# Performance work log

Measured on AMD Instinct MI355X. Metric: run time of the kernel, lower is better.

Reference implementation:

```python
import jax, jax.numpy as jnp
import numpy as np
from jax import lax

B, T = 16, 1000
IN_DIM = 257
CTX = 3            # left + 1 + right
FEAT = CTX * IN_DIM  # 771
H = 512
L = 2              # SRU layers
KN = 9             # conv kernels
KS = 6             # conv kernel size


def setup_inputs() -> dict:
    key = jax.random.key(0)
    ks = jax.random.split(key, 10)
    n = jax.random.normal
    return {
        "inputs": n(ks[0], (B, T, FEAT), jnp.float32),
        "W_in": n(ks[1], (FEAT, H), jnp.float32) / np.sqrt(FEAT),
        "b_in": jnp.zeros((H,), jnp.float32),
        "W_rnn": n(ks[2], (L, H, 3 * H), jnp.float32) / np.sqrt(H),
        "v_rnn": n(ks[3], (L, 2 * H), jnp.float32) * 0.1,
        "b_rnn": jnp.zeros((L, 2 * H), jnp.float32),
        "conv_k": n(ks[4], (KN, 1, KS, KS), jnp.float32) * 0.05,
        "conv_b": jnp.zeros((KN,), jnp.float32),
        "W_out": n(ks[5], (H * KN, FEAT), jnp.float32) / np.sqrt(H * KN),
        "b_out": jnp.zeros((FEAT,), jnp.float32),
    }


def _sru_layer(x, W, v, b):
    # x: (T, B, H) time-major; SRU: c_t = f_t*c_{t-1} + (1-f_t)*(W x_t),
    # highway h_t = r_t*c_t + (1-r_t)*x_t; gates peek at c_{t-1} via v.
    U = jnp.einsum("tbh,hk->tbk", x, W)          # (T, B, 3H)
    xt, fp, rp = jnp.split(U, 3, axis=-1)
    vf, vr = jnp.split(v, 2)
    bf, br = jnp.split(b, 2)

    def step(c, inp):
        xt_t, fp_t, rp_t, xin_t = inp
        f = jax.nn.sigmoid(fp_t + vf * c + bf)
        c_new = f * c + (1.0 - f) * xt_t
        r = jax.nn.sigmoid(rp_t + vr * c + br)
        h = r * c_new + (1.0 - r) * xin_t
        return c_new, h

    c0 = jnp.zeros(x.shape[1:], x.dtype)
    _, hs = lax.scan(step, c0, (xt, fp, rp, x))
    return hs


def reference(inputs, W_in, b_in, W_rnn, v_rnn, b_rnn, conv_k, conv_b, W_out, b_out):
    # input layer: Linear + Tanh
    h = jnp.tanh(jnp.einsum("btf,fh->bth", inputs, W_in) + b_in)  # (B,T,H)
    x = jnp.transpose(h, (1, 0, 2))                               # (T,B,H)
    for l in range(L):
        x = _sru_layer(x, W_rnn[l], v_rnn[l], b_rnn[l])
    h = jnp.transpose(x, (1, 0, 2))[:, None]                      # (B,1,T,H)

    # Conv2d with asymmetric pad (left/top 3, right/bottom 2), +bias, tanh
    y = lax.conv_general_dilated(
        h, conv_k, window_strides=(1, 1), padding=[(3, 2), (3, 2)],
        dimension_numbers=("NCHW", "OIHW", "NCHW"))
    y = jnp.tanh(y + conv_b[None, :, None, None])                 # (B,KN,T,H)
    # MaxPool2d(3, stride=1, padding=1)
    y = lax.reduce_window(y, -jnp.inf, lax.max, (1, 1, 3, 3), (1, 1, 1, 1),
                          [(0, 0), (0, 0), (1, 1), (1, 1)])

    # (B,KN,T,H) -> (B,T,H,KN) -> (B,T,H*KN)  (matches torch double transpose)
    y = jnp.transpose(y, (0, 2, 3, 1)).reshape(B, T, H * KN)
    mask = jax.nn.sigmoid(jnp.einsum("btf,fo->bto", y, W_out) + b_out)
    out = mask * inputs
    return out[:, :, IN_DIM:2 * IN_DIM]  # center frame (left_context slice)
```

## Files before the change

kernel.cpp:

```cpp
#include <hip/hip_runtime.h>
#include <hip/hip_bf16.h>

#define B_    16
#define T_    1000
#define FEAT  771
#define FEATP 800
#define H_    512
#define H3    1536
#define KN_   9
#define KHID  4608
#define M_    16000
#define NOUT  257
#define KSLICES 3

typedef _Float16 half8 __attribute__((ext_vector_type(8)));
typedef _Float16 half4 __attribute__((ext_vector_type(4)));
typedef _Float16 half2v __attribute__((ext_vector_type(2)));
typedef _Float16 h2 __attribute__((ext_vector_type(2)));
typedef float    floatx4 __attribute__((ext_vector_type(4)));

__device__ inline float tanh_fast(float z) {
    return 1.0f - 2.0f / (1.0f + __expf(2.0f * z));
}
__device__ inline float sigmoid_fast(float z) {
    return 1.0f / (1.0f + __expf(-z));
}

__device__ inline void gload16(const _Float16* g, _Float16* l) {
    __builtin_amdgcn_global_load_lds(
        (const __attribute__((address_space(1))) void*)g,
        (__attribute__((address_space(3))) void*)l, 16, 0, 0);
}

__device__ inline h2 pkfma(unsigned int w, unsigned int x, h2 c) {
    const h2 a = __builtin_bit_cast(h2, w);
    const h2 b = __builtin_bit_cast(h2, x);
#if __has_builtin(__builtin_elementwise_fma)
    return __builtin_elementwise_fma(a, b, c);
#else
    return a * b + c;
#endif
}

__global__ void convert_inputs(const float* __restrict__ in, _Float16* __restrict__ A1) {
    size_t i = (size_t)blockIdx.x * 256 + threadIdx.x;
    if (i >= (size_t)M_ * FEATP) return;
    size_t r = i / FEATP;
    int   cc = (int)(i % FEATP);
    A1[i] = (cc < FEAT) ? (_Float16)in[r * FEAT + cc] : (_Float16)0.f;
}

__global__ void pack_ck(const float* __restrict__ ck, unsigned int* __restrict__ ckp) {
    const int i = threadIdx.x;
    if (i < 9 * 36) {
        const _Float16 w = (_Float16)ck[i];
        const unsigned short u = __builtin_bit_cast(unsigned short, w);
        ckp[i] = ((unsigned int)u << 16) | u;
    }
}

__global__ __launch_bounds__(256) void transpose_w(
    const float* __restrict__ W, _Float16* __restrict__ Wt,
    int K, int N, int ldw, int coloff, int Kp, int perm9)
{
    __shared__ float tile[32][33];
    const int kb = blockIdx.x * 32;
    const int nb = blockIdx.y * 32;
    const int tx = threadIdx.x & 31;
    const int ty = threadIdx.x >> 5;
    #pragma unroll
    for (int r = ty; r < 32; r += 8) {
        const int k = kb + r, n = nb + tx;
        tile[r][tx] = (k < K && n < N) ? W[(size_t)k * ldw + coloff + n] : 0.f;
    }
    __syncthreads();
    #pragma unroll
    for (int r = ty; r < 32; r += 8) {
        const int n = nb + r, k = kb + tx;
        if (n < N && k < Kp) {
            size_t kidx = (size_t)k;
            if (perm9) kidx = (size_t)(k % 9) * 512 + (size_t)(k / 9);
            Wt[(size_t)n * Kp + kidx] = (_Float16)tile[tx][r];
        }
    }
}

template <int EPI>
__global__ __launch_bounds__(256) void gemm_kernel(
    const _Float16* __restrict__ A, const _Float16* __restrict__ Bt,
    int Kp, int nk, int Nb,
    _Float16* __restrict__ Ch, float* __restrict__ Cf, int ldc,
    const float* __restrict__ bias)
{
    __shared__ __align__(16) _Float16 As[128][32];
    __shared__ __align__(16) _Float16 Bs[128][32];

    const int tid  = threadIdx.x;
    const int m0   = blockIdx.x * 128;
    const int n0   = blockIdx.y * 128;
    const int koff = blockIdx.z * (nk << 5);
    const int wave = tid >> 6;
    const int lane = tid & 63;
    const int wr   = (wave >> 1) << 6;
    const int wc   = (wave & 1) << 6;
    const int lrow = lane & 15;
    const int lq   = lane >> 4;

    const int srow0  = wave * 32 + (lane >> 2);
    const int schunk = (lane & 3) * 8;
    const _Float16* aSrc = A  + (size_t)(m0 + srow0) * Kp + koff + schunk;
    const _Float16* bSrc = Bt + (size_t)(n0 + srow0) * Kp + koff + schunk;
    _Float16* aDst0 = &As[wave * 32][0];
    _Float16* aDst1 = &As[wave * 32 + 16][0];
    _Float16* bDst0 = &Bs[wave * 32][0];
    _Float16* bDst1 = &Bs[wave * 32 + 16][0];
    const size_t rstep = (size_t)16 * Kp;

    floatx4 acc[4][4];
    #pragma unroll
    for (int i = 0; i < 4; ++i)
        #pragma unroll
        for (int j = 0; j < 4; ++j)
            #pragma unroll
            for (int r = 0; r < 4; ++r) acc[i][j][r] = 0.f;

    for (int kc = 0; kc < nk; ++kc) {
        __syncthreads();
        gload16(aSrc,         aDst0);
        gload16(aSrc + rstep, aDst1);
        gload16(bSrc,         bDst0);
        gload16(bSrc + rstep, bDst1);
        aSrc += 32; bSrc += 32;
        __syncthreads();

        half8 af[4], bfr[4];
        #pragma unroll
        for (int i = 0; i < 4; ++i) af[i]  = *(const half8*)(&As[wr + i * 16 + lrow][lq * 8]);
        #pragma unroll
        for (int j = 0; j < 4; ++j) bfr[j] = *(const half8*)(&Bs[wc + j * 16 + lrow][lq * 8]);
        #pragma unroll
        for (int i = 0; i < 4; ++i)
            #pragma unroll
            for (int j = 0; j < 4; ++j)
                acc[i][j] = __builtin_amdgcn_mfma_f32_16x16x32_f16(af[i], bfr[j], acc[i][j], 0, 0, 0);
    }

    #pragma unroll
    for (int j = 0; j < 4; ++j) {
        const int col = n0 + wc + j * 16 + lrow;
        if (col >= Nb) continue;
        #pragma unroll
        for (int i = 0; i < 4; ++i) {
            #pragma unroll
            for (int r = 0; r < 4; ++r) {
                const int row = m0 + wr + i * 16 + lq * 4 + r;
                float v = acc[i][j][r];
                if constexpr (EPI == 0) {
                    float z = v + bias[col];
                    Ch[(size_t)row * ldc + col] = (_Float16)tanh_fast(z);
                } else if constexpr (EPI == 1) {
                    Ch[(size_t)(col >> 9) * ((size_t)M_ * 512) + (size_t)row * 512 + (col & 511)] = (_Float16)v;
                } else {
                    Cf[(size_t)blockIdx.z * M_ * NOUT + (size_t)row * NOUT + col] = v;
                }
            }
        }
    }
}

__global__ __launch_bounds__(256) void reduce_out(
    const float* __restrict__ Cp, const float* __restrict__ bias,
    const float* __restrict__ aux, float* __restrict__ out)
{
    const size_t i = (size_t)blockIdx.x * 256 + threadIdx.x;
    if (i >= (size_t)M_ * NOUT) return;
    const int row = (int)(i / NOUT);
    const int col = (int)(i % NOUT);
    float s = Cp[i] + Cp[i + (size_t)M_ * NOUT] + Cp[i + 2 * (size_t)M_ * NOUT];
    out[i] = sigmoid_fast(s + bias[col]) * aux[(size_t)row * FEAT + 257 + col];
}

__global__ __launch_bounds__(256) void repack_u(
    const _Float16* __restrict__ U,
    const _Float16* __restrict__ X,
    _Float16* __restrict__ Upk)
{
    const size_t i = (size_t)blockIdx.x * 256 + threadIdx.x;
    if (i >= (size_t)M_ * 128) return;
    const size_t base = i << 2;
    const half4 a = *(const half4*)(U + base);
    const half4 f = *(const half4*)(U + (size_t)M_ * 512 + base);
    const half4 r = *(const half4*)(U + 2 * (size_t)M_ * 512 + base);
    const half4 x = *(const half4*)(X + base);
    half8 lo, hi;
    lo[0] = a[0]; lo[1] = f[0]; lo[2] = r[0]; lo[3] = x[0];
    lo[4] = a[1]; lo[5] = f[1]; lo[6] = r[1]; lo[7] = x[1];
    hi[0] = a[2]; hi[1] = f[2]; hi[2] = r[2]; hi[3] = x[2];
    hi[4] = a[3]; hi[5] = f[3]; hi[6] = r[3]; hi[7] = x[3];
    *(half8*)(Upk + base * 4)     = lo;
    *(half8*)(Upk + base * 4 + 8) = hi;
}

__global__ __launch_bounds__(64) void sru_scan(
    const _Float16* __restrict__ Upk, _Float16* __restrict__ Xout,
    const float* __restrict__ v, const float* __restrict__ bg)
{
    const int gid = blockIdx.x * 64 + threadIdx.x;
    const int b = gid >> 9;
    const int h = gid & 511;
    const float vf = v[h],      vr = v[512 + h];
    const float bf = bg[h],     br = bg[512 + h];

    const _Float16* p = Upk + ((size_t)b * T_ * 512 + h) * 4;
    _Float16* ox = Xout + (size_t)b * T_ * 512 + h;

    half4 buf[20];
    #pragma unroll
    for (int j = 0; j < 20; ++j) buf[j] = *(const half4*)(p + (size_t)j * 2048);

    float c = 0.f;
    for (int t0 = 0; t0 < T_; t0 += 20) {
        #pragma unroll
        for (int j = 0; j < 20; ++j) {
            const int t = t0 + j;
            const half4 cur = buf[j];
            const int tn = t + 20;
            if (tn < T_) buf[j] = *(const half4*)(p + (size_t)tn * 2048);
            const float xt = (float)cur[0];
            const float fp = (float)cur[1];
            const float rp = (float)cur[2];
            const float x  = (float)cur[3];
            const float f  = sigmoid_fast(fp + vf * c + bf);
            const float r  = sigmoid_fast(rp + vr * c + br);
            const float cn = f * c + (1.0f - f) * xt;
            const float hO = r * cn + (1.0f - r) * x;
            ox[(size_t)t * 512] = (_Float16)hO;
            c = cn;
        }
    }
}

#define CVW 76

__global__ __launch_bounds__(320) void conv_pool(
    const _Float16* __restrict__ X, const unsigned int* __restrict__ ckp,
    const float* __restrict__ cb, _Float16* __restrict__ A3)
{
    __shared__ __align__(16) _Float16 in_s[23][80];
    __shared__ __align__(16) _Float16 cv[9][18][CVW];
    const int tid = threadIdx.x;
    int bi = blockIdx.x;
    const int th = bi & 7;  bi >>= 3;
    const int tt = bi % 63;
    const int b  = bi / 63;
    const int t0 = tt * 16, h0 = th * 64;

    for (int i = tid; i < 23 * 76; i += 320) {
        const int r = i / 76, cc = i % 76;
        const int gt = t0 - 4 + r, gh = h0 - 4 + cc;
        _Float16 val = (_Float16)0.f;
        if (gt >= 0 && gt < T_ && gh >= 0 && gh < H_)
            val = X[((size_t)b * T_ + gt) * H_ + gh];
        in_s[r][cc] = val;
    }
    __syncthreads();

    if (tid < 306) {
        const int pt = tid / 17;
        const int co = (tid % 17) * 4;

        const int ct = t0 - 1 + pt;
        const bool rok = (ct >= 0) && (ct < T_);
        const int chb = h0 - 1 + co;
        const bool ok0 = rok && (chb + 0 >= 0) && (chb + 0 < H_);
        const bool ok1 = rok && (chb + 1 >= 0) && (chb + 1 < H_);
        const bool ok2 = rok && (chb + 2 >= 0) && (chb + 2 < H_);
        const bool ok3 = rok && (chb + 3 >= 0) && (chb + 3 < H_);

        h2 acc0[9], acc1[9];
        #pragma unroll
        for (int k = 0; k < 9; ++k) {
            acc0[k][0] = (_Float16)0.f; acc0[k][1] = (_Float16)0.f;
            acc1[k][0] = (_Float16)0.f; acc1[k][1] = (_Float16)0.f;
        }

        #pragma unroll 1
        for (int ii = 0; ii < 6; ++ii) {
            const unsigned int* rw = (const unsigned int*)&in_s[pt + ii][co];
            const uint2 a01 = *(const uint2*)(rw);
            const uint2 a23 = *(const uint2*)(rw + 2);
            const unsigned int A0 = a01.x, A1v = a01.y, A2 = a23.x, A3v = a23.y;
            const unsigned int A4 = rw[4];
            const unsigned int M0 = (A0  >> 16) | (A1v << 16);
            const unsigned int M1 = (A1v >> 16) | (A2  << 16);
            const unsigned int M2 = (A2  >> 16) | (A3v << 16);
            const unsigned int M3 = (A3v >> 16) | (A4  << 16);

            const unsigned int* wt = ckp + ii * 6;
            #pragma unroll
            for (int k = 0; k < 9; ++k) {
                const unsigned int* wk = wt + k * 36;
                acc0[k] = pkfma(wk[0], A0,  acc0[k]);  acc1[k] = pkfma(wk[0], A1v, acc1[k]);
                acc0[k] = pkfma(wk[1], M0,  acc0[k]);  acc1[k] = pkfma(wk[1], M1,  acc1[k]);
                acc0[k] = pkfma(wk[2], A1v, acc0[k]);  acc1[k] = pkfma(wk[2], A2,  acc1[k]);
                acc0[k] = pkfma(wk[3], M1,  acc0[k]);  acc1[k] = pkfma(wk[3], M2,  acc1[k]);
                acc0[k] = pkfma(wk[4], A2,  acc0[k]);  acc1[k] = pkfma(wk[4], A3v, acc1[k]);
                acc0[k] = pkfma(wk[5], M2,  acc0[k]);  acc1[k] = pkfma(wk[5], M3,  acc1[k]);
            }
        }

        const _Float16 NEG = (_Float16)(-65504.f);
        #pragma unroll
        for (int k = 0; k < 9; ++k) {
            half4 o;
            o[0] = ok0 ? acc0[k][0] : NEG;
            o[1] = ok1 ? acc0[k][1] : NEG;
            o[2] = ok2 ? acc1[k][0] : NEG;
            o[3] = ok3 ? acc1[k][1] : NEG;
            *(half4*)(&cv[k][pt][co]) = o;
        }
    }
    __syncthreads();

    if (tid < 256) {
        const int pt = tid >> 4;
        const int gt = t0 + pt;
        if (gt < T_) {
            const int ph = (tid & 15) * 4;
            _Float16* dst = A3 + ((size_t)b * T_ + gt) * KHID + (h0 + ph);
            #pragma unroll
            for (int k = 0; k < 9; ++k) {
                float q0 = -1e30f, q1 = -1e30f, q2 = -1e30f, q3 = -1e30f;
                #pragma unroll
                for (int dr = 0; dr < 3; ++dr) {
                    const _Float16* cr = &cv[k][pt + dr][ph];
                    const half4  a = *(const half4*)(cr);
                    const half2v bq = *(const half2v*)(cr + 4);
                    const float v0 = (float)a[0], v1 = (float)a[1], v2 = (float)a[2];
                    const float v3 = (float)a[3], v4 = (float)bq[0], v5 = (float)bq[1];
                    const float t01 = fmaxf(v1, v2);
                    const float t34 = fmaxf(v3, v4);
                    q0 = fmaxf(q0, fmaxf(v0, t01));
                    q1 = fmaxf(q1, fmaxf(t01, v3));
                    q2 = fmaxf(q2, fmaxf(v2, t34));
                    q3 = fmaxf(q3, fmaxf(t34, v5));
                }
                const float bk = cb[k];
                half4 o;
                o[0] = (_Float16)tanh_fast(q0 + bk);
                o[1] = (_Float16)tanh_fast(q1 + bk);
                o[2] = (_Float16)tanh_fast(q2 + bk);
                o[3] = (_Float16)tanh_fast(q3 + bk);
                *(half4*)(dst + (size_t)k * 512) = o;
            }
        }
    }
}

extern "C" void kernel_launch(void* const* d_in, const int* in_sizes, int n_in,
                              void* d_out, int out_size, void* d_ws, size_t ws_size,
                              hipStream_t stream) {
    const float* inputs = (const float*)d_in[0];
    const float* W_in   = (const float*)d_in[1];
    const float* b_in   = (const float*)d_in[2];
    const float* W_rnn  = (const float*)d_in[3];
    const float* v_rnn  = (const float*)d_in[4];
    const float* b_rnn  = (const float*)d_in[5];
    const float* conv_k = (const float*)d_in[6];
    const float* conv_b = (const float*)d_in[7];
    const float* W_out  = (const float*)d_in[8];
    const float* b_out  = (const float*)d_in[9];
    float* out = (float*)d_out;

    char* ws = (char*)d_ws;
    size_t off = 0;
    auto take = [&](size_t bytes) -> char* {
        off = (off + 255) & ~(size_t)255;
        char* p = ws + off;
        off += bytes;
        return p;
    };
    _Float16* W3T  = (_Float16*)take((size_t)NOUT * KHID * 2);
    _Float16* A1   = (_Float16*)take((size_t)M_ * FEATP * 2);
    _Float16* W1T  = (_Float16*)take((size_t)H_ * FEATP * 2);
    _Float16* W2T0 = (_Float16*)take((size_t)H3 * H_ * 2);
    _Float16* W2T1 = (_Float16*)take((size_t)H3 * H_ * 2);
    _Float16* X0   = (_Float16*)take((size_t)M_ * H_ * 2);
    _Float16* X1   = (_Float16*)take((size_t)M_ * H_ * 2);
    _Float16* U    = (_Float16*)take(3 * (size_t)M_ * 512 * 2);
    _Float16* A3   = (_Float16*)take((size_t)M_ * KHID * 2);
    unsigned int* ckp = (unsigned int*)take(9 * 36 * 4);
    _Float16* Upk = A3;
    float* Cp = (float*)A1;
    _Float16* X2 = X0;

    {
        size_t n = (size_t)M_ * FEATP;
        convert_inputs<<<dim3((unsigned)((n + 255) / 256)), 256, 0, stream>>>(inputs, A1);
    }
    pack_ck<<<dim3(1), 384, 0, stream>>>(conv_k, ckp);
    transpose_w<<<dim3(25, 16), 256, 0, stream>>>(W_in, W1T, FEAT, H_, H_, 0, FEATP, 0);
    transpose_w<<<dim3(16, 48), 256, 0, stream>>>(W_rnn, W2T0, H_, H3, H3, 0, H_, 0);
    transpose_w<<<dim3(16, 48), 256, 0, stream>>>(W_rnn + (size_t)H_ * H3, W2T1, H_, H3, H3, 0, H_, 0);
    transpose_w<<<dim3(144, 9), 256, 0, stream>>>(W_out, W3T, KHID, NOUT, FEAT, 257, KHID, 1);

    const unsigned nrep = (unsigned)(((size_t)M_ * 128 + 255) / 256);

    gemm_kernel<0><<<dim3(125, 4), 256, 0, stream>>>(A1, W1T, FEATP, 25, H_, X0, nullptr, H_, b_in);

    gemm_kernel<1><<<dim3(125, 12), 256, 0, stream>>>(X0, W2T0, H_, 16, H3, U, nullptr, 0, nullptr);
    repack_u<<<dim3(nrep), 256, 0, stream>>>(U, X0, Upk);
    sru_scan<<<dim3(128), 64, 0, stream>>>(Upk, X1, v_rnn, b_rnn);

    gemm_kernel<1><<<dim3(125, 12), 256, 0, stream>>>(X1, W2T1, H_, 16, H3, U, nullptr, 0, nullptr);
    repack_u<<<dim3(nrep), 256, 0, stream>>>(U, X1, Upk);
    sru_scan<<<dim3(128), 64, 0, stream>>>(Upk, X2, v_rnn + 1024, b_rnn + 1024);

    conv_pool<<<dim3(16 * 63 * 8), 320, 0, stream>>>(X2, ckp, conv_b, A3);

    gemm_kernel<3><<<dim3(125, 3, KSLICES), 256, 0, stream>>>(A3, W3T, KHID, 144 / KSLICES, NOUT, nullptr, Cp, 0, nullptr);
    {
        const unsigned nred = (unsigned)(((size_t)M_ * NOUT + 255) / 256);
        reduce_out<<<dim3(nred), 256, 0, stream>>>(Cp, b_out + 257, inputs, out);
    }
}
```

Before: 816.2 us.

## Double-buffer GEMM LDS tiles and use packed-f16 asm in conv and maxpool

The GEMM kernel now keeps two LDS buffers, so the next K-slice streams in through global_load_lds while MFMAs run on the current one. This cuts the barriers per iteration from two to one. The conv kernel uses inline v_pk_fma_f16 asm with scalar weight operands and alignbit for the half-word shifts. The maxpool is redone with packed f16 max instead of per-element float max. The GEMM change doubles LDS use, and the 's' asm constraint on loaded weights may force readfirstlane or uniform-load handling.

```diff
diff --git a/kernel.cpp b/kernel.cpp
--- a/kernel.cpp
+++ b/kernel.cpp
@@ -32,14 +32,13 @@
         (__attribute__((address_space(3))) void*)l, 16, 0, 0);
 }
 
-__device__ inline h2 pkfma(unsigned int w, unsigned int x, h2 c) {
-    const h2 a = __builtin_bit_cast(h2, w);
-    const h2 b = __builtin_bit_cast(h2, x);
-#if __has_builtin(__builtin_elementwise_fma)
-    return __builtin_elementwise_fma(a, b, c);
-#else
-    return a * b + c;
-#endif
+__device__ inline void pk_fma_acc(unsigned& acc, unsigned w, unsigned x) {
+    asm("v_pk_fma_f16 %0, %1, %2, %0" : "+v"(acc) : "s"(w), "v"(x));
+}
+__device__ inline unsigned pk_max(unsigned a, unsigned b) {
+    unsigned d;
+    asm("v_pk_max_f16 %0, %1, %2" : "=v"(d) : "v"(a), "v"(b));
+    return d;
 }
 
 __global__ void convert_inputs(const float* __restrict__ in, _Float16* __restrict__ A1) {
@@ -92,8 +91,8 @@
     _Float16* __restrict__ Ch, float* __restrict__ Cf, int ldc,
     const float* __restrict__ bias)
 {
-    __shared__ __align__(16) _Float16 As[128][32];
-    __shared__ __align__(16) _Float16 Bs[128][32];
+    __shared__ __align__(16) _Float16 As[2][128][32];
+    __shared__ __align__(16) _Float16 Bs[2][128][32];
 
     const int tid  = threadIdx.x;
     const int m0   = blockIdx.x * 128;
@@ -110,10 +109,6 @@
     const int schunk = (lane & 3) * 8;
     const _Float16* aSrc = A  + (size_t)(m0 + srow0) * Kp + koff + schunk;
     const _Float16* bSrc = Bt + (size_t)(n0 + srow0) * Kp + koff + schunk;
-    _Float16* aDst0 = &As[wave * 32][0];
-    _Float16* aDst1 = &As[wave * 32 + 16][0];
-    _Float16* bDst0 = &Bs[wave * 32][0];
-    _Float16* bDst1 = &Bs[wave * 32 + 16][0];
     const size_t rstep = (size_t)16 * Kp;
 
     floatx4 acc[4][4];
@@ -124,25 +119,39 @@
             #pragma unroll
             for (int r = 0; r < 4; ++r) acc[i][j][r] = 0.f;
 
+    gload16(aSrc,         &As[0][wave * 32][0]);
+    gload16(aSrc + rstep, &As[0][wave * 32 + 16][0]);
+    gload16(bSrc,         &Bs[0][wave * 32][0]);
+    gload16(bSrc + rstep, &Bs[0][wave * 32 + 16][0]);
+    asm volatile("s_waitcnt vmcnt(0)" ::: "memory");
+    __builtin_amdgcn_s_barrier();
+
     for (int kc = 0; kc < nk; ++kc) {
-        __syncthreads();
-        gload16(aSrc,         aDst0);
-        gload16(aSrc + rstep, aDst1);
-        gload16(bSrc,         bDst0);
-        gload16(bSrc + rstep, bDst1);
-        aSrc += 32; bSrc += 32;
-        __syncthreads();
+        const int cur = kc & 1;
+        if (kc + 1 < nk) {
+            const _Float16* a2 = aSrc + (size_t)(kc + 1) * 32;
+            const _Float16* b2 = bSrc + (size_t)(kc + 1) * 32;
+            gload16(a2,         &As[cur ^ 1][wave * 32][0]);
+            gload16(a2 + rstep, &As[cur ^ 1][wave * 32 + 16][0]);
+            gload16(b2,         &Bs[cur ^ 1][wave * 32][0]);
+            gload16(b2 + rstep, &Bs[cur ^ 1][wave * 32 + 16][0]);
+        }
 
         half8 af[4], bfr[4];
         #pragma unroll
-        for (int i = 0; i < 4; ++i) af[i]  = *(const half8*)(&As[wr + i * 16 + lrow][lq * 8]);
-        #pragma unroll
-        for (int j = 0; j < 4; ++j) bfr[j] = *(const half8*)(&Bs[wc + j * 16 + lrow][lq * 8]);
+        for (int i = 0; i < 4; ++i) af[i]  = *(const half8*)(&As[cur][wr + i * 16 + lrow][lq * 8]);
+        #pragma unroll
+        for (int j = 0; j < 4; ++j) bfr[j] = *(const half8*)(&Bs[cur][wc + j * 16 + lrow][lq * 8]);
         #pragma unroll
         for (int i = 0; i < 4; ++i)
             #pragma unroll
             for (int j = 0; j < 4; ++j)
                 acc[i][j] = __builtin_amdgcn_mfma_f32_16x16x32_f16(af[i], bfr[j], acc[i][j], 0, 0, 0);
+
+        if (kc + 1 < nk) {
+            asm volatile("s_waitcnt vmcnt(0)" ::: "memory");
+            __builtin_amdgcn_s_barrier();
+        }
     }
 
     #pragma unroll
@@ -277,12 +286,9 @@
         const bool ok2 = rok && (chb + 2 >= 0) && (chb + 2 < H_);
         const bool ok3 = rok && (chb + 3 >= 0) && (chb + 3 < H_);
 
-        h2 acc0[9], acc1[9];
-        #pragma unroll
-        for (int k = 0; k < 9; ++k) {
-            acc0[k][0] = (_Float16)0.f; acc0[k][1] = (_Float16)0.f;
-            acc1[k][0] = (_Float16)0.f; acc1[k][1] = (_Float16)0.f;
-        }
+        unsigned acc0[9], acc1[9];
+        #pragma unroll
+        for (int k = 0; k < 9; ++k) { acc0[k] = 0u; acc1[k] = 0u; }
 
         #pragma unroll 1
         for (int ii = 0; ii < 6; ++ii) {
@@ -291,32 +297,34 @@
             const uint2 a23 = *(const uint2*)(rw + 2);
             const unsigned int A0 = a01.x, A1v = a01.y, A2 = a23.x, A3v = a23.y;
             const unsigned int A4 = rw[4];
-            const unsigned int M0 = (A0  >> 16) | (A1v << 16);
-            const unsigned int M1 = (A1v >> 16) | (A2  << 16);
-            const unsigned int M2 = (A2  >> 16) | (A3v << 16);
-            const unsigned int M3 = (A3v >> 16) | (A4  << 16);
+            const unsigned int M0 = __builtin_amdgcn_alignbit(A1v, A0, 16);
+            const unsigned int M1 = __builtin_amdgcn_alignbit(A2, A1v, 16);
+            const unsigned int M2 = __builtin_amdgcn_alignbit(A3v, A2, 16);
+            const unsigned int M3 = __builtin_amdgcn_alignbit(A4, A3v, 16);
 
             const unsigned int* wt = ckp + ii * 6;
             #pragma unroll
             for (int k = 0; k < 9; ++k) {
                 const unsigned int* wk = wt + k * 36;
-                acc0[k] = pkfma(wk[0], A0,  acc0[k]);  acc1[k] = pkfma(wk[0], A1v, acc1[k]);
-                acc0[k] = pkfma(wk[1], M0,  acc0[k]);  acc1[k] = pkfma(wk[1], M1,  acc1[k]);
-                acc0[k] = pkfma(wk[2], A1v, acc0[k]);  acc1[k] = pkfma(wk[2], A2,  acc1[k]);
-                acc0[k] = pkfma(wk[3], M1,  acc0[k]);  acc1[k] = pkfma(wk[3], M2,  acc1[k]);
-                acc0[k] = pkfma(wk[4], A2,  acc0[k]);  acc1[k] = pkfma(wk[4], A3v, acc1[k]);
-                acc0[k] = pkfma(wk[5], M2,  acc0[k]);  acc1[k] = pkfma(wk[5], M3,  acc1[k]);
+                pk_fma_acc(acc0[k], wk[0], A0);   pk_fma_acc(acc1[k], wk[0], A1v);
+                pk_fma_acc(acc0[k], wk[1], M0);   pk_fma_acc(acc1[k], wk[1], M1);
+                pk_fma_acc(acc0[k], wk[2], A1v);  pk_fma_acc(acc1[k], wk[2], A2);
+                pk_fma_acc(acc0[k], wk[3], M1);   pk_fma_acc(acc1[k], wk[3], M2);
+                pk_fma_acc(acc0[k], wk[4], A2);   pk_fma_acc(acc1[k], wk[4], A3v);
+                pk_fma_acc(acc0[k], wk[5], M2);   pk_fma_acc(acc1[k], wk[5], M3);
             }
         }
 
         const _Float16 NEG = (_Float16)(-65504.f);
         #pragma unroll
         for (int k = 0; k < 9; ++k) {
+            const h2 pa = __builtin_bit_cast(h2, acc0[k]);
+            const h2 pb = __builtin_bit_cast(h2, acc1[k]);
             half4 o;
-            o[0] = ok0 ? acc0[k][0] : NEG;
-            o[1] = ok1 ? acc0[k][1] : NEG;
-            o[2] = ok2 ? acc1[k][0] : NEG;
-            o[3] = ok3 ? acc1[k][1] : NEG;
+            o[0] = ok0 ? pa[0] : NEG;
+            o[1] = ok1 ? pa[1] : NEG;
+            o[2] = ok2 ? pb[0] : NEG;
+            o[3] = ok3 ? pb[1] : NEG;
             *(half4*)(&cv[k][pt][co]) = o;
         }
     }
@@ -330,27 +338,25 @@
             _Float16* dst = A3 + ((size_t)b * T_ + gt) * KHID + (h0 + ph);
             #pragma unroll
             for (int k = 0; k < 9; ++k) {
-                float q0 = -1e30f, q1 = -1e30f, q2 = -1e30f, q3 = -1e30f;
+                unsigned q01 = 0xFC00FC00u, q23 = 0xFC00FC00u;
                 #pragma unroll
                 for (int dr = 0; dr < 3; ++dr) {
-                    const _Float16* cr = &cv[k][pt + dr][ph];
-                    const half4  a = *(const half4*)(cr);
-                    const half2v bq = *(const half2v*)(cr + 4);
-                    const float v0 = (float)a[0], v1 = (float)a[1], v2 = (float)a[2];
-                    const float v3 = (float)a[3], v4 = (float)bq[0], v5 = (float)bq[1];
-                    const float t01 = fmaxf(v1, v2);
-                    const float t34 = fmaxf(v3, v4);
-                    q0 = fmaxf(q0, fmaxf(v0, t01));
-                    q1 = fmaxf(q1, fmaxf(t01, v3));
-                    q2 = fmaxf(q2, fmaxf(v2, t34));
-                    q3 = fmaxf(q3, fmaxf(t34, v5));
+                    const unsigned* cr = (const unsigned*)&cv[k][pt + dr][ph];
+                    const uint2 w01 = *(const uint2*)(cr);
+                    const unsigned w2 = cr[2];
+                    const unsigned m12 = __builtin_amdgcn_alignbit(w01.y, w01.x, 16);
+                    const unsigned m34 = __builtin_amdgcn_alignbit(w2, w01.y, 16);
+                    q01 = pk_max(q01, pk_max(pk_max(w01.x, m12), w01.y));
+                    q23 = pk_max(q23, pk_max(pk_max(w01.y, m34), w2));
                 }
+                const h2 qa = __builtin_bit_cast(h2, q01);
+                const h2 qb = __builtin_bit_cast(h2, q23);
                 const float bk = cb[k];
                 half4 o;
-                o[0] = (_Float16)tanh_fast(q0 + bk);
-                o[1] = (_Float16)tanh_fast(q1 + bk);
-                o[2] = (_Float16)tanh_fast(q2 + bk);
-                o[3] = (_Float16)tanh_fast(q3 + bk);
+                o[0] = (_Float16)tanh_fast((float)qa[0] + bk);
+                o[1] = (_Float16)tanh_fast((float)qa[1] + bk);
+                o[2] = (_Float16)tanh_fast((float)qb[0] + bk);
+                o[3] = (_Float16)tanh_fast((float)qb[1] + bk);
                 *(half4*)(dst + (size_t)k * 512) = o;
             }
         }
```

Result: no change. 803.1 us (-1.6%).
